# Performance work log

Hardware: AMD Instinct MI355X
Metric: run time of the kernel (lower is better)

The kernel has to match this reference:

```python
import jax, jax.numpy as jnp
import numpy as np

# Daubechies-2 (db2) filter bank coefficients, as in pywt.Wavelet('db2')
_DEC_LO = np.array([-0.12940952255126037, 0.22414386804185735, 0.8365163037378079, 0.48296291314453416], dtype=np.float32)
_DEC_HI = np.array([-0.48296291314453416, 0.8365163037378079, -0.22414386804185735, -0.12940952255126037], dtype=np.float32)
_REC_LO = _DEC_LO[::-1].copy()
_REC_HI = _DEC_HI[::-1].copy()
_FLEN = 4


def _conv_valid(x, h):
    # np.convolve(x, h, 'valid') along last axis (true convolution: filter flipped)
    F = h.shape[0]
    N = x.shape[-1]
    hf = h[::-1]
    out = hf[0] * x[..., 0:N - F + 1]
    for k in range(1, F):
        out = out + hf[k] * x[..., k:N - F + 1 + k]
    return out


def dwt_db2(x):
    # pywt.dwt(x, 'db2') with default symmetric mode, axis=-1. x: (B, N) -> (B, (N+3)//2) x2
    xe = jnp.pad(x, ((0, 0), (_FLEN - 1, _FLEN - 1)), mode='symmetric')
    lo = jnp.asarray(_DEC_LO, dtype=x.dtype)
    hi = jnp.asarray(_DEC_HI, dtype=x.dtype)
    cA = _conv_valid(xe, lo)[..., 1::2]
    cD = _conv_valid(xe, hi)[..., 1::2]
    return cA, cD


def idwt_db2(cA, cD):
    # pywt.idwt(cA, cD, 'db2'): upsample-by-2 (len 2L-1), full conv with rec filters,
    # trim (flen-2) each side == pad by 1 and valid conv. Output length 2L - flen + 2.
    L = cA.shape[-1]
    def up(c):
        u = jnp.zeros(c.shape[:-1] + (2 * L - 1,), dtype=c.dtype)
        return u.at[..., ::2].set(c)
    uA = jnp.pad(up(cA), ((0, 0), (1, 1)))
    uD = jnp.pad(up(cD), ((0, 0), (1, 1)))
    rlo = jnp.asarray(_REC_LO, dtype=cA.dtype)
    rhi = jnp.asarray(_REC_HI, dtype=cA.dtype)
    return _conv_valid(uA, rlo) + _conv_valid(uD, rhi)


def setup_inputs() -> dict:
    key = jax.random.key(0)
    k1, k2 = jax.random.split(key)
    B, N = 4096, 4096
    output_dim = (N + 3) // 2  # 2049
    x = jax.random.normal(k1, (B, N), dtype=jnp.float32)
    # keras 'uniform' initializer: U(-0.05, 0.05), shape (input_shape[1], output_dim)
    kernel = jax.random.uniform(k2, (N, output_dim), dtype=jnp.float32, minval=-0.05, maxval=0.05)
    return {"x": x, "kernel": kernel}


def reference(x, kernel):
    cA, cD = dwt_db2(x)            # (B, L)
    cA = cA * kernel               # learned multiplicative gain
    cD = cD * kernel
    y = idwt_db2(cA, cD)           # (B, 2L - 2) == (B, N)
    return jax.nn.relu(y)
```

## Files before the change

kernel.cpp:

```cpp
#include <hip/hip_runtime.h>


#define NN 4096
#define LL 2049
#define PAIRS4 1024

__global__ __launch_bounds__(256) void wavelet_fused(const float* __restrict__ x,
                                                     const float* __restrict__ ker,
                                                     float* __restrict__ out) {
    const int row = blockIdx.y;
    const int t   = blockIdx.x * 256 + threadIdx.x;

    const float lo0 = -0.12940952255126037f, lo1 = 0.22414386804185735f,
                lo2 =  0.8365163037378079f,  lo3 = 0.48296291314453416f;
    const float hi0 = -0.48296291314453416f, hi1 = 0.8365163037378079f,
                hi2 = -0.22414386804185735f, hi3 = -0.12940952255126037f;

    const float4* x4 = (const float4*)(x + (size_t)row * NN);

    const int tp = (t == 0) ? 0 : (t - 1);
    const int tn = (t == PAIRS4 - 1) ? t : (t + 1);
    const float4 vp = x4[tp];
    const float4 vc = x4[t];
    const float4 vn = x4[tn];

    const bool first = (t == 0);
    const bool last  = (t == PAIRS4 - 1);
    const float e0 = first ? vc.y : vp.z;
    const float e1 = first ? vc.x : vp.w;
    const float e2 = vc.x;
    const float e3 = vc.y;
    const float e4 = vc.z;
    const float e5 = vc.w;
    const float e6 = last ? vc.w : vn.x;
    const float e7 = last ? vc.z : vn.y;

    const float* krow = ker + (size_t)row * LL;
    const float g0 = krow[2 * t];
    const float g1 = krow[2 * t + 1];
    const float g2 = krow[2 * t + 2];

    const float cA0 = lo3 * e0 + lo2 * e1 + lo1 * e2 + lo0 * e3;
    const float cD0 = hi3 * e0 + hi2 * e1 + hi1 * e2 + hi0 * e3;
    const float cA1 = lo3 * e2 + lo2 * e3 + lo1 * e4 + lo0 * e5;
    const float cD1 = hi3 * e2 + hi2 * e3 + hi1 * e4 + hi0 * e5;
    const float cA2 = lo3 * e4 + lo2 * e5 + lo1 * e6 + lo0 * e7;
    const float cD2 = hi3 * e4 + hi2 * e5 + hi1 * e6 + hi0 * e7;

    const float A0 = g0 * cA0, D0 = g0 * cD0;
    const float A1 = g1 * cA1, D1 = g1 * cD1;
    const float A2 = g2 * cA2, D2 = g2 * cD2;

    float y0 = lo1 * A0 + lo3 * A1 + hi1 * D0 + hi3 * D1;
    float y1 = lo0 * A0 + lo2 * A1 + hi0 * D0 + hi2 * D1;
    float y2 = lo1 * A1 + lo3 * A2 + hi1 * D1 + hi3 * D2;
    float y3 = lo0 * A1 + lo2 * A2 + hi0 * D1 + hi2 * D2;

    y0 = fmaxf(y0, 0.0f);
    y1 = fmaxf(y1, 0.0f);
    y2 = fmaxf(y2, 0.0f);
    y3 = fmaxf(y3, 0.0f);

    float4* out4 = (float4*)(out + (size_t)row * NN);
    out4[t] = make_float4(y0, y1, y2, y3);
}

extern "C" void kernel_launch(void* const* d_in, const int* in_sizes, int n_in,
                              void* d_out, int out_size, void* d_ws, size_t ws_size,
                              hipStream_t stream) {
    const float* x   = (const float*)d_in[0];
    const float* ker = (const float*)d_in[1];
    float* out = (float*)d_out;
    wavelet_fused<<<dim3(PAIRS4 / 256, 4096), dim3(256), 0, stream>>>(x, ker, out);
}
```

Baseline: 136.8 us.

## Stage each row's signal and gain in shared memory with one block per row

Each row is now handled by a single 1024-thread block. The block first loads the whole signal row and the kernel gain row into LDS with coalesced loads, then reads its neighbouring float4s and gain values from LDS. This removes the redundant, partly misaligned global loads of neighbour vectors and the unaligned scalar gain loads. The cost is a block-wide barrier and about 24KB of LDS per block, which can limit occupancy and the overlap between loads and compute.

```diff
diff --git a/kernel.cpp b/kernel.cpp
--- a/kernel.cpp
+++ b/kernel.cpp
@@ -3,13 +3,15 @@
 
 #define NN 4096
 #define LL 2049
-#define PAIRS4 1024
 
-__global__ __launch_bounds__(256) void wavelet_fused(const float* __restrict__ x,
-                                                     const float* __restrict__ ker,
-                                                     float* __restrict__ out) {
-    const int row = blockIdx.y;
-    const int t   = blockIdx.x * 256 + threadIdx.x;
+__global__ __launch_bounds__(1024) void wavelet_fused(const float* __restrict__ x,
+                                                      const float* __restrict__ ker,
+                                                      float* __restrict__ out) {
+    __shared__ float s_x[NN];
+    __shared__ float s_g[LL];
+
+    const int row = blockIdx.x;
+    const int i   = threadIdx.x;
 
     const float lo0 = -0.12940952255126037f, lo1 = 0.22414386804185735f,
                 lo2 =  0.8365163037378079f,  lo3 = 0.48296291314453416f;
@@ -17,28 +19,27 @@
                 hi2 = -0.22414386804185735f, hi3 = -0.12940952255126037f;
 
     const float4* x4 = (const float4*)(x + (size_t)row * NN);
+    ((float4*)s_x)[i] = x4[i];
+    const float* krow = ker + (size_t)row * LL;
+    s_g[i]        = krow[i];
+    s_g[i + 1024] = krow[i + 1024];
+    if (i == 0) s_g[2048] = krow[2048];
+    __syncthreads();
 
-    const int tp = (t == 0) ? 0 : (t - 1);
-    const int tn = (t == PAIRS4 - 1) ? t : (t + 1);
-    const float4 vp = x4[tp];
-    const float4 vc = x4[t];
-    const float4 vn = x4[tn];
+    const bool first = (i == 0);
+    const bool last  = (i == 1023);
+    const float4 L = *(const float4*)(s_x + (first ? 0 : 4 * i - 4));
+    const float4 C = *(const float4*)(s_x + 4 * i);
+    const float4 R = *(const float4*)(s_x + (last ? 4092 : 4 * i + 4));
 
-    const bool first = (t == 0);
-    const bool last  = (t == PAIRS4 - 1);
-    const float e0 = first ? vc.y : vp.z;
-    const float e1 = first ? vc.x : vp.w;
-    const float e2 = vc.x;
-    const float e3 = vc.y;
-    const float e4 = vc.z;
-    const float e5 = vc.w;
-    const float e6 = last ? vc.w : vn.x;
-    const float e7 = last ? vc.z : vn.y;
+    const float e0 = first ? L.y : L.z;
+    const float e1 = first ? L.x : L.w;
+    const float e2 = C.x, e3 = C.y, e4 = C.z, e5 = C.w;
+    const float e6 = last ? R.w : R.x;
+    const float e7 = last ? R.z : R.y;
 
-    const float* krow = ker + (size_t)row * LL;
-    const float g0 = krow[2 * t];
-    const float g1 = krow[2 * t + 1];
-    const float g2 = krow[2 * t + 2];
+    const float2 gp = *(const float2*)(s_g + 2 * i);
+    const float  g2 = s_g[2 * i + 2];
 
     const float cA0 = lo3 * e0 + lo2 * e1 + lo1 * e2 + lo0 * e3;
     const float cD0 = hi3 * e0 + hi2 * e1 + hi1 * e2 + hi0 * e3;
@@ -47,22 +48,21 @@
     const float cA2 = lo3 * e4 + lo2 * e5 + lo1 * e6 + lo0 * e7;
     const float cD2 = hi3 * e4 + hi2 * e5 + hi1 * e6 + hi0 * e7;
 
-    const float A0 = g0 * cA0, D0 = g0 * cD0;
-    const float A1 = g1 * cA1, D1 = g1 * cD1;
-    const float A2 = g2 * cA2, D2 = g2 * cD2;
+    const float A0 = gp.x * cA0, D0 = gp.x * cD0;
+    const float A1 = gp.y * cA1, D1 = gp.y * cD1;
+    const float A2 = g2   * cA2, D2 = g2   * cD2;
 
     float y0 = lo1 * A0 + lo3 * A1 + hi1 * D0 + hi3 * D1;
     float y1 = lo0 * A0 + lo2 * A1 + hi0 * D0 + hi2 * D1;
     float y2 = lo1 * A1 + lo3 * A2 + hi1 * D1 + hi3 * D2;
     float y3 = lo0 * A1 + lo2 * A2 + hi0 * D1 + hi2 * D2;
-
     y0 = fmaxf(y0, 0.0f);
     y1 = fmaxf(y1, 0.0f);
     y2 = fmaxf(y2, 0.0f);
     y3 = fmaxf(y3, 0.0f);
 
     float4* out4 = (float4*)(out + (size_t)row * NN);
-    out4[t] = make_float4(y0, y1, y2, y3);
+    out4[i] = make_float4(y0, y1, y2, y3);
 }
 
 extern "C" void kernel_launch(void* const* d_in, const int* in_sizes, int n_in,
@@ -71,5 +71,5 @@
     const float* x   = (const float*)d_in[0];
     const float* ker = (const float*)d_in[1];
     float* out = (float*)d_out;
-    wavelet_fused<<<dim3(PAIRS4 / 256, 4096), dim3(256), 0, stream>>>(x, ker, out);
+    wavelet_fused<<<dim3(4096), dim3(1024), 0, stream>>>(x, ker, out);
 }
```

Result: no change. 139.1 us (+1.7%).
